# Kernel tuning notes

Measured on AMD Instinct MI355X. Metric: run time of the kernel, lower is better.

The kernel has to match this reference:

```python
import jax, jax.numpy as jnp
import numpy as np

N_NODES = 100000
N_EDGES = 600000
EMB_DIM = 128
NUM_LAYER = 3
NUM_GRAPHS = 64


def setup_inputs() -> dict:
    key = jax.random.key(0)
    ks = jax.random.split(key, 10)
    s = 1.0 / np.sqrt(EMB_DIM)  # keep activations stable through stacked GEMMs
    return {
        "x": jax.random.randint(ks[0], (N_NODES, 2), 0, 2),
        "edge_index_pos": jax.random.randint(ks[1], (2, N_EDGES), 0, N_NODES),
        "edge_index_inv": jax.random.randint(ks[2], (2, N_EDGES), 0, N_NODES),
        "batch": jnp.sort(jax.random.randint(ks[3], (N_NODES,), 0, NUM_GRAPHS)),
        "type_emb": jax.random.normal(ks[4], (14, EMB_DIM), jnp.float32),
        "output_emb": jax.random.normal(ks[5], (2, EMB_DIM), jnp.float32),
        "lin1_w": jax.random.normal(ks[6], (NUM_LAYER, 2, EMB_DIM, EMB_DIM), jnp.float32) * s,
        "lin1_b": jnp.zeros((NUM_LAYER, 2, EMB_DIM), jnp.float32),
        "lin2_w": jax.random.normal(ks[7], (NUM_LAYER, 2, EMB_DIM, EMB_DIM), jnp.float32) * s,
        "lin2_b": jnp.zeros((NUM_LAYER, 2, EMB_DIM), jnp.float32),
    }


def _gin_rel(h, ei, w1, b1, w2, b2):
    # GINConv (eps=0): MLP(x + sum_{j in N(i)} x_j); messages flow src(row0)->dst(row1)
    agg = jax.ops.segment_sum(h[ei[0]], ei[1], num_segments=h.shape[0])
    z = jax.nn.relu((h + agg) @ w1 + b1)
    return z @ w2 + b2


def reference(x, edge_index_pos, edge_index_inv, batch, type_emb, output_emb,
              lin1_w, lin1_b, lin2_w, lin2_b):
    # node input embedding: type + output-flag
    h = type_emb[x[:, 0]] + output_emb[x[:, 1]]
    num_layer = lin1_w.shape[0]
    for l in range(num_layer):  # small fixed layer loop
        hn = (_gin_rel(h, edge_index_pos, lin1_w[l, 0], lin1_b[l, 0], lin2_w[l, 0], lin2_b[l, 0])
              + _gin_rel(h, edge_index_inv, lin1_w[l, 1], lin1_b[l, 1], lin2_w[l, 1], lin2_b[l, 1]))
        h = hn if l == num_layer - 1 else jax.nn.relu(hn)  # JK='last', drop_ratio=0
    node_rep = h
    # MultiAggregation(['sum','mean','max','min']) pooling by graph id
    sum_g = jax.ops.segment_sum(node_rep, batch, num_segments=NUM_GRAPHS)
    cnt = jax.ops.segment_sum(jnp.ones((node_rep.shape[0],), node_rep.dtype), batch, num_segments=NUM_GRAPHS)
    mean_g = sum_g / jnp.maximum(cnt, 1.0)[:, None]
    max_g = jax.ops.segment_max(node_rep, batch, num_segments=NUM_GRAPHS)
    min_g = jax.ops.segment_min(node_rep, batch, num_segments=NUM_GRAPHS)
    h_graph = jnp.concatenate([sum_g, mean_g, max_g, min_g], axis=1)  # [B, 4*D]
    h_graph = h_graph.reshape(NUM_GRAPHS, -1, 4).transpose(0, 2, 1)   # [B, 4, D] (interleaved as in torch view)
    batch_mask = jnp.ones((NUM_GRAPHS, 4), dtype=bool)
    return (h_graph, batch_mask)
```

## Files before the change

kernel.cpp:

```cpp
#include <hip/hip_runtime.h>
#include <stdint.h>

#define M_NODES 100000
#define M_PAD   100096
#define NE      600000
#define DIM     128
#define NGRAPH  64
#define SCAN_B  512
#define SCAN_NB ((M_NODES + SCAN_B - 1) / SCAN_B)
#define WP      136

typedef __attribute__((ext_vector_type(8))) short short8;
typedef __attribute__((ext_vector_type(4))) float f32x4;

__device__ inline float bf2lo(uint32_t u) { return __uint_as_float(u << 16); }
__device__ inline float bf2hi(uint32_t u) { return __uint_as_float(u & 0xffff0000u); }
__device__ inline uint32_t packbf2(float a, float b) {
    uint32_t ua = __float_as_uint(a), ub = __float_as_uint(b);
    ua += 0x7fffu + ((ua >> 16) & 1u);
    ub += 0x7fffu + ((ub >> 16) & 1u);
    return (ua >> 16) | (ub & 0xffff0000u);
}
__device__ inline uint16_t ftobf16(float f) {
    uint32_t u = __float_as_uint(f);
    u += 0x7fffu + ((u >> 16) & 1u);
    return (uint16_t)(u >> 16);
}

#define GB_EMBED 25000
#define GB_TRANS (GB_EMBED + 12)
#define GB_ZERO  (GB_TRANS + 391)
#define GB_BOUND (GB_ZERO + 391)
__global__ void k_setup(const int* __restrict__ x, const float2* __restrict__ te2,
                        const float2* __restrict__ oe2, uint32_t* __restrict__ h2,
                        const float* __restrict__ w1, const float* __restrict__ w2,
                        uint16_t* __restrict__ wfrag,
                        const int* __restrict__ batch, int* __restrict__ starts,
                        int* __restrict__ degp, int* __restrict__ degi,
                        int* __restrict__ curp, int* __restrict__ curi) {
    int b = blockIdx.x, t = threadIdx.x;
    if (b < GB_EMBED) {
        int id = b * 256 + t;
        int node = id >> 6, p = id & 63;
        int x0 = x[node * 2], x1 = x[node * 2 + 1];
        float2 a = te2[x0 * 64 + p], bb = oe2[x1 * 64 + p];
        h2[node * 64 + p] = packbf2(a.x + bb.x, a.y + bb.y);
    } else if (b < GB_TRANS) {
        int m = b - GB_EMBED;
        const float* src;
        uint16_t* dst;
        if (m < 6) {
            int L = m >> 1, rel = m & 1;
            src = w1 + m * 16384;
            dst = wfrag + (size_t)(L * 4 + rel) * 16384;
        } else {
            int mm = m - 6, L = mm >> 1, rel = mm & 1;
            src = w2 + mm * 16384;
            dst = wfrag + (size_t)(L * 4 + 2 + rel) * 16384;
        }
        for (int o = t; o < 16384; o += 256) {
            int f = o >> 3, j = o & 7;
            int fb = f >> 6, ln = f & 63;
            int t_ = fb >> 2, s_ = fb & 3, qq = ln >> 4, ll = ln & 15;
            dst[o] = ftobf16(src[(s_ * 32 + qq * 8 + j) * 128 + t_ * 16 + ll]);
        }
    } else if (b < GB_ZERO) {
        int i = (b - GB_TRANS) * 256 + t;
        if (i < M_NODES) { degp[i] = 0; degi[i] = 0; curp[i] = 0; curi[i] = 0; }
    } else {
        int i = (b - GB_ZERO) * 256 + t;
        if (i >= M_NODES) return;
        int bb = batch[i];
        int pb = (i == 0) ? -1 : batch[i - 1];
        for (int g = pb + 1; g <= bb; ++g) starts[g] = i;
        if (i == M_NODES - 1)
            for (int g = bb + 1; g <= NGRAPH; ++g) starts[g] = M_NODES;
    }
}

__global__ void k_hist(const int* __restrict__ ep, const int* __restrict__ ei,
                       int* __restrict__ degp, int* __restrict__ degi) {
    int e = blockIdx.x * blockDim.x + threadIdx.x;
    if (e >= NE) return;
    atomicAdd(&degp[ep[NE + e]], 1);
    atomicAdd(&degi[ei[NE + e]], 1);
}

__global__ void k_scan1(const int* __restrict__ degp, const int* __restrict__ degi,
                        int* __restrict__ rsp, int* __restrict__ rsi, int* __restrict__ bsum) {
    __shared__ int s[SCAN_B];
    int list = blockIdx.y;
    const int* deg = list ? degi : degp;
    int* rs = list ? rsi : rsp;
    int i = blockIdx.x * SCAN_B + threadIdx.x;
    int v = (i < M_NODES) ? deg[i] : 0;
    s[threadIdx.x] = v;
    __syncthreads();
    for (int off = 1; off < SCAN_B; off <<= 1) {
        int xv = (threadIdx.x >= off) ? s[threadIdx.x - off] : 0;
        __syncthreads();
        s[threadIdx.x] += xv;
        __syncthreads();
    }
    if (i < M_NODES) rs[i + 1] = s[threadIdx.x];
    if (threadIdx.x == SCAN_B - 1) bsum[list * SCAN_NB + blockIdx.x] = s[threadIdx.x];
}

__global__ void k_scan2(const int* __restrict__ bsum, int* __restrict__ boff) {
    __shared__ int s[256];
    int list = blockIdx.x, t = threadIdx.x;
    int v = (t < SCAN_NB) ? bsum[list * SCAN_NB + t] : 0;
    s[t] = v;
    __syncthreads();
    for (int off = 1; off < 256; off <<= 1) {
        int xv = (t >= off) ? s[t - off] : 0;
        __syncthreads();
        s[t] += xv;
        __syncthreads();
    }
    if (t < SCAN_NB) boff[list * SCAN_NB + t] = s[t] - v;
}

__global__ void k_scan3(int* __restrict__ rsp, int* __restrict__ rsi, const int* __restrict__ boff) {
    int list = blockIdx.y;
    int* rs = list ? rsi : rsp;
    int i = blockIdx.x * SCAN_B + threadIdx.x;
    if (i < M_NODES) rs[i + 1] += boff[list * SCAN_NB + blockIdx.x];
    if (i == 0 && list == 0) { rsp[0] = 0; rsi[0] = 0; }
}

__global__ void k_fill(const int* __restrict__ ep, const int* __restrict__ ei,
                       const int* __restrict__ rsp, const int* __restrict__ rsi,
                       int* __restrict__ curp, int* __restrict__ curi,
                       int* __restrict__ csrp, int* __restrict__ csri) {
    int e = blockIdx.x * blockDim.x + threadIdx.x;
    if (e >= NE) return;
    int dp = ep[NE + e], sp_ = ep[e];
    int di = ei[NE + e], si_ = ei[e];
#pragma unroll 1
    for (int w = 0; w < 8; ++w) {
        int lo = w * 12500, hi = lo + 12500;
        if (dp >= lo && dp < hi) { int p = atomicAdd(&curp[dp], 1); csrp[rsp[dp] + p] = sp_; }
        if (di >= lo && di < hi) { int p = atomicAdd(&curi[di], 1); csri[rsi[di] + p] = si_; }
    }
}

__device__ inline void add8(float* a, uint4 v) {
    a[0] += bf2lo(v.x); a[1] += bf2hi(v.x);
    a[2] += bf2lo(v.y); a[3] += bf2hi(v.y);
    a[4] += bf2lo(v.z); a[5] += bf2hi(v.z);
    a[6] += bf2lo(v.w); a[7] += bf2hi(v.w);
}

__device__ inline void gather_tail(const uint4* __restrict__ h4, const int* __restrict__ csr,
                                   int e, int e1, int p, float* a) {
    for (; e + 4 <= e1; e += 4) {
        int i0 = csr[e], i1 = csr[e + 1], i2 = csr[e + 2], i3 = csr[e + 3];
        uint4 v0 = h4[(size_t)i0 * 16 + p];
        uint4 v1 = h4[(size_t)i1 * 16 + p];
        uint4 v2 = h4[(size_t)i2 * 16 + p];
        uint4 v3 = h4[(size_t)i3 * 16 + p];
        add8(a, v0); add8(a, v1); add8(a, v2); add8(a, v3);
    }
    for (; e < e1; ++e) add8(a, h4[(size_t)csr[e] * 16 + p]);
}

__global__ void k_aggregate2(const uint4* __restrict__ h4,
                             const int* __restrict__ rsp, const int* __restrict__ csrp,
                             const int* __restrict__ rsi, const int* __restrict__ csri,
                             uint4* __restrict__ up, uint4* __restrict__ ui) {
    int id = blockIdx.x * blockDim.x + threadIdx.x;
    int node = id >> 4, p = id & 15;
    if (node >= M_NODES) return;
    uint4 hv = h4[(size_t)node * 16 + p];
    float a[8] = {bf2lo(hv.x), bf2hi(hv.x), bf2lo(hv.y), bf2hi(hv.y),
                  bf2lo(hv.z), bf2hi(hv.z), bf2lo(hv.w), bf2hi(hv.w)};
    float b[8];
#pragma unroll
    for (int j = 0; j < 8; ++j) b[j] = a[j];
    int ea = rsp[node], e1a = rsp[node + 1];
    int eb = rsi[node], e1b = rsi[node + 1];
    while (ea + 2 <= e1a && eb + 2 <= e1b) {
        int ia0 = csrp[ea], ia1 = csrp[ea + 1];
        int ib0 = csri[eb], ib1 = csri[eb + 1];
        uint4 va0 = h4[(size_t)ia0 * 16 + p];
        uint4 va1 = h4[(size_t)ia1 * 16 + p];
        uint4 vb0 = h4[(size_t)ib0 * 16 + p];
        uint4 vb1 = h4[(size_t)ib1 * 16 + p];
        add8(a, va0); add8(a, va1); add8(b, vb0); add8(b, vb1);
        ea += 2; eb += 2;
    }
    gather_tail(h4, csrp, ea, e1a, p, a);
    gather_tail(h4, csri, eb, e1b, p, b);
    up[(size_t)node * 16 + p] = make_uint4(packbf2(a[0], a[1]), packbf2(a[2], a[3]),
                                           packbf2(a[4], a[5]), packbf2(a[6], a[7]));
    ui[(size_t)node * 16 + p] = make_uint4(packbf2(b[0], b[1]), packbf2(b[2], b[3]),
                                           packbf2(b[4], b[5]), packbf2(b[6], b[7]));
}

__launch_bounds__(256, 2)
__global__ void k_gemm2(const uint16_t* __restrict__ Up, const uint16_t* __restrict__ Ui,
                        const uint16_t* __restrict__ WF1p, const float* __restrict__ B1p,
                        const uint16_t* __restrict__ WF2p, const float* __restrict__ B2p,
                        const uint16_t* __restrict__ WF1i, const float* __restrict__ B1i,
                        const uint16_t* __restrict__ WF2i, const float* __restrict__ B2i,
                        float* __restrict__ HN, uint16_t* __restrict__ HOUT, int last) {
    __shared__ __align__(16) uint16_t wbuf[16384];
    __shared__ __align__(16) uint16_t sZ[2][64 * WP];
    int tid = threadIdx.x;
    int wave = tid >> 6, lane = tid & 63;
    int q = lane >> 4, l16 = lane & 15;
    int rb0 = blockIdx.x * 128 + wave * 16;
    int rb1 = rb0 + 64;

    auto loadA = [&](const uint16_t* U, int rowbase, short8* v) {
        const uint16_t* P = U + (size_t)(rowbase + l16) * DIM + q * 8;
#pragma unroll
        for (int s = 0; s < 4; ++s) v[s] = *(const short8*)(P + s * 32);
    };
    auto loadw = [&](const uint16_t* WF) {
#pragma unroll
        for (int i = tid; i < 2048; i += 256)
            *(uint4*)&wbuf[i * 8] = *(const uint4*)(WF + (size_t)i * 8);
    };
    auto stage1 = [&](const short8* af, const float* B1, int zslot) {
        f32x4 acc1[8];
#pragma unroll
        for (int t = 0; t < 8; ++t) acc1[t] = (f32x4){0.f, 0.f, 0.f, 0.f};
#pragma unroll
        for (int t = 0; t < 8; ++t)
#pragma unroll
            for (int s = 0; s < 4; ++s) {
                short8 bb = *(const short8*)&wbuf[((t * 4 + s) * 64 + lane) * 8];
                acc1[t] = __builtin_amdgcn_mfma_f32_16x16x32_bf16(af[s], bb, acc1[t], 0, 0, 0);
            }
#pragma unroll
        for (int t = 0; t < 8; ++t) {
            float b1v = B1[t * 16 + l16];
#pragma unroll
            for (int r = 0; r < 4; ++r)
                sZ[zslot][(wave * 16 + q * 4 + r) * WP + t * 16 + l16] =
                    ftobf16(fmaxf(acc1[t][r] + b1v, 0.f));
        }
    };
    auto stage2 = [&](int zslot, f32x4* acc2) {
        short8 zf[4];
#pragma unroll
        for (int s = 0; s < 4; ++s)
            zf[s] = *(const short8*)&sZ[zslot][(wave * 16 + l16) * WP + s * 32 + q * 8];
#pragma unroll
        for (int t = 0; t < 8; ++t)
#pragma unroll
            for (int s = 0; s < 4; ++s) {
                short8 bb = *(const short8*)&wbuf[((t * 4 + s) * 64 + lane) * 8];
                acc2[t] = __builtin_amdgcn_mfma_f32_16x16x32_bf16(zf[s], bb, acc2[t], 0, 0, 0);
            }
    };

    f32x4 acc2a[8], acc2b[8];
#pragma unroll
    for (int t = 0; t < 8; ++t) { acc2a[t] = (f32x4){0.f,0.f,0.f,0.f}; acc2b[t] = (f32x4){0.f,0.f,0.f,0.f}; }

    short8 af0[4], af1[4];
    loadA(Up, rb0, af0); loadA(Up, rb1, af1);
    loadw(WF1p); __syncthreads();
    stage1(af0, B1p, 0); stage1(af1, B1p, 1);
    __syncthreads();
    loadw(WF2p); __syncthreads();
    stage2(0, acc2a); stage2(1, acc2b);
    __syncthreads();
    loadA(Ui, rb0, af0); loadA(Ui, rb1, af1);
    loadw(WF1i); __syncthreads();
    stage1(af0, B1i, 0); stage1(af1, B1i, 1);
    __syncthreads();
    loadw(WF2i); __syncthreads();
    stage2(0, acc2a); stage2(1, acc2b);

#pragma unroll
    for (int t = 0; t < 8; ++t) {
        int col = t * 16 + l16;
        float b2v = B2p[col] + B2i[col];
#pragma unroll
        for (int r = 0; r < 4; ++r) {
            int row0 = rb0 + q * 4 + r, row1 = rb1 + q * 4 + r;
            float y0 = acc2a[t][r] + b2v, y1 = acc2b[t][r] + b2v;
            if (last) {
                HN[(size_t)row0 * DIM + col] = y0;
                HN[(size_t)row1 * DIM + col] = y1;
            } else {
                HOUT[(size_t)row0 * DIM + col] = ftobf16(fmaxf(y0, 0.f));
                HOUT[(size_t)row1 * DIM + col] = ftobf16(fmaxf(y1, 0.f));
            }
        }
    }
}

__global__ void k_pool1(const float* __restrict__ HN, const int* __restrict__ starts,
                        float* __restrict__ psum, float* __restrict__ pmax, float* __restrict__ pmin) {
    int g = blockIdx.x, sp = blockIdx.y, t = threadIdx.x;
    int d = t & 127, rh = t >> 7;
    int slot = sp * 2 + rh;
    int s0 = starts[g], s1 = starts[g + 1];
    float s = 0.f, mx = -INFINITY, mn = INFINITY;
    for (int i = s0 + slot; i < s1; i += 32) {
        float v = HN[(size_t)i * DIM + d];
        s += v; mx = fmaxf(mx, v); mn = fminf(mn, v);
    }
    int o = (g * 32 + slot) * DIM + d;
    psum[o] = s; pmax[o] = mx; pmin[o] = mn;
}

__global__ void k_pool2(const float* __restrict__ psum, const float* __restrict__ pmax,
                        const float* __restrict__ pmin, const int* __restrict__ starts,
                        float* __restrict__ out) {
    __shared__ float S[4][128];
    int g = blockIdx.x, t = threadIdx.x;
    float s = 0.f, mx = -INFINITY, mn = INFINITY;
    for (int p = 0; p < 32; ++p) {
        int o = (g * 32 + p) * DIM + t;
        s += psum[o]; mx = fmaxf(mx, pmax[o]); mn = fminf(mn, pmin[o]);
    }
    float cnt = (float)(starts[g + 1] - starts[g]);
    float mean = s / fmaxf(cnt, 1.f);
    S[0][t] = s; S[1][t] = mean; S[2][t] = mx; S[3][t] = mn;
    __syncthreads();
#pragma unroll
    for (int k = 0; k < 4; ++k) {
        int j = 4 * t + k;
        out[g * 512 + k * 128 + t] = S[j >> 7][j & 127];
    }
    if (t < 4) out[NGRAPH * 512 + g * 4 + t] = 1.0f;
}

extern "C" void kernel_launch(void* const* d_in, const int* in_sizes, int n_in,
                              void* d_out, int out_size, void* d_ws, size_t ws_size,
                              hipStream_t stream) {
    const int* x     = (const int*)d_in[0];
    const int* ep    = (const int*)d_in[1];
    const int* ei    = (const int*)d_in[2];
    const int* batch = (const int*)d_in[3];
    const float* te  = (const float*)d_in[4];
    const float* oe  = (const float*)d_in[5];
    const float* w1  = (const float*)d_in[6];
    const float* b1  = (const float*)d_in[7];
    const float* w2  = (const float*)d_in[8];
    const float* b2  = (const float*)d_in[9];
    float* out = (float*)d_out;

    char* w = (char*)d_ws;
    auto alloc = [&](size_t n) { char* p = w; w += (n + 255) & ~(size_t)255; return p; };
    uint16_t* h_bf  = (uint16_t*)alloc((size_t)M_PAD * DIM * 2);
    uint16_t* u_pos = (uint16_t*)alloc((size_t)M_PAD * DIM * 2);
    uint16_t* u_inv = (uint16_t*)alloc((size_t)M_PAD * DIM * 2);
    float*    hn    = (float*)alloc((size_t)M_PAD * DIM * 4);
    uint16_t* wfrag = (uint16_t*)alloc((size_t)12 * 16384 * 2);
    int* rsp  = (int*)alloc((M_NODES + 2) * 4);
    int* rsi  = (int*)alloc((M_NODES + 2) * 4);
    int* degp = (int*)alloc(M_NODES * 4);
    int* degi = (int*)alloc(M_NODES * 4);
    int* curp = (int*)alloc(M_NODES * 4);
    int* curi = (int*)alloc(M_NODES * 4);
    int* csrp = (int*)alloc((size_t)NE * 4);
    int* csri = (int*)alloc((size_t)NE * 4);
    int* bsum = (int*)alloc(2 * SCAN_NB * 4);
    int* boff = (int*)alloc(2 * SCAN_NB * 4);
    int* starts = (int*)alloc((NGRAPH + 1) * 4);
    float* psum = (float*)alloc(NGRAPH * 32 * DIM * 4);
    float* pmax = (float*)alloc(NGRAPH * 32 * DIM * 4);
    float* pmin = (float*)alloc(NGRAPH * 32 * DIM * 4);
    if ((size_t)(w - (char*)d_ws) > ws_size) return;

    k_setup<<<GB_BOUND, 256, 0, stream>>>(x, (const float2*)te, (const float2*)oe,
                                          (uint32_t*)h_bf, w1, w2, wfrag,
                                          batch, starts, degp, degi, curp, curi);
    k_hist<<<(NE + 255) / 256, 256, 0, stream>>>(ep, ei, degp, degi);
    dim3 gs(SCAN_NB, 2);
    k_scan1<<<gs, SCAN_B, 0, stream>>>(degp, degi, rsp, rsi, bsum);
    k_scan2<<<2, 256, 0, stream>>>(bsum, boff);
    k_scan3<<<gs, SCAN_B, 0, stream>>>(rsp, rsi, boff);
    k_fill<<<(NE + 255) / 256, 256, 0, stream>>>(ep, ei, rsp, rsi, curp, curi, csrp, csri);

    for (int l = 0; l < 3; ++l) {
        k_aggregate2<<<(M_NODES * 16 + 255) / 256, 256, 0, stream>>>(
            (const uint4*)h_bf, rsp, csrp, rsi, csri, (uint4*)u_pos, (uint4*)u_inv);
        const uint16_t* wfL = wfrag + (size_t)l * 4 * 16384;
        k_gemm2<<<M_PAD / 128, 256, 0, stream>>>(
            u_pos, u_inv,
            wfL,              b1 + (2 * l) * 128,
            wfL + 2 * 16384,  b2 + (2 * l) * 128,
            wfL + 16384,      b1 + (2 * l + 1) * 128,
            wfL + 3 * 16384,  b2 + (2 * l + 1) * 128,
            hn, h_bf, (l == 2) ? 1 : 0);
    }
    dim3 gp(NGRAPH, 16);
    k_pool1<<<gp, 256, 0, stream>>>(hn, starts, psum, pmax, pmin);
    k_pool2<<<NGRAPH, 128, 0, stream>>>(psum, pmax, pmin, starts, out);
}
```

Before: 543.4 us.

## Double-buffer GEMM weights in LDS and stage output stores through shared memory

The fused two-relation MLP kernel now prefetches the next weight matrix into registers while the current MFMA stage runs, then commits it to a second LDS buffer. This halves the number of barriers and hides the global weight loads. Output writes are also routed through LDS so each lane stores contiguous 16-byte vectors instead of scattered 2- or 4-byte elements. The extra LDS buffer and 32 prefetch registers lead to lowering the launch-bounds occupancy hint from 2 to 1, which may reduce latency hiding.

```diff
diff --git a/kernel.cpp b/kernel.cpp
--- a/kernel.cpp
+++ b/kernel.cpp
@@ -198,14 +198,14 @@
                                            packbf2(b[4], b[5]), packbf2(b[6], b[7]));
 }
 
-__launch_bounds__(256, 2)
+__launch_bounds__(256, 1)
 __global__ void k_gemm2(const uint16_t* __restrict__ Up, const uint16_t* __restrict__ Ui,
                         const uint16_t* __restrict__ WF1p, const float* __restrict__ B1p,
                         const uint16_t* __restrict__ WF2p, const float* __restrict__ B2p,
                         const uint16_t* __restrict__ WF1i, const float* __restrict__ B1i,
                         const uint16_t* __restrict__ WF2i, const float* __restrict__ B2i,
                         float* __restrict__ HN, uint16_t* __restrict__ HOUT, int last) {
-    __shared__ __align__(16) uint16_t wbuf[16384];
+    __shared__ __align__(16) uint16_t wbuf[2][16384];
     __shared__ __align__(16) uint16_t sZ[2][64 * WP];
     int tid = threadIdx.x;
     int wave = tid >> 6, lane = tid & 63;
@@ -213,17 +213,23 @@
     int rb0 = blockIdx.x * 128 + wave * 16;
     int rb1 = rb0 + 64;
 
+    uint4 pf[8];
+    auto issueW = [&](const uint16_t* WF) {
+#pragma unroll
+        for (int i = 0; i < 8; ++i)
+            pf[i] = *(const uint4*)(WF + (size_t)(tid + i * 256) * 8);
+    };
+    auto commitW = [&](int wb) {
+#pragma unroll
+        for (int i = 0; i < 8; ++i)
+            *(uint4*)&wbuf[wb][(size_t)(tid + i * 256) * 8] = pf[i];
+    };
     auto loadA = [&](const uint16_t* U, int rowbase, short8* v) {
         const uint16_t* P = U + (size_t)(rowbase + l16) * DIM + q * 8;
 #pragma unroll
         for (int s = 0; s < 4; ++s) v[s] = *(const short8*)(P + s * 32);
     };
-    auto loadw = [&](const uint16_t* WF) {
-#pragma unroll
-        for (int i = tid; i < 2048; i += 256)
-            *(uint4*)&wbuf[i * 8] = *(const uint4*)(WF + (size_t)i * 8);
-    };
-    auto stage1 = [&](const short8* af, const float* B1, int zslot) {
+    auto stage1 = [&](const short8* af, const float* B1, int zslot, int wb) {
         f32x4 acc1[8];
 #pragma unroll
         for (int t = 0; t < 8; ++t) acc1[t] = (f32x4){0.f, 0.f, 0.f, 0.f};
@@ -231,7 +237,7 @@
         for (int t = 0; t < 8; ++t)
 #pragma unroll
             for (int s = 0; s < 4; ++s) {
-                short8 bb = *(const short8*)&wbuf[((t * 4 + s) * 64 + lane) * 8];
+                short8 bb = *(const short8*)&wbuf[wb][((t * 4 + s) * 64 + lane) * 8];
                 acc1[t] = __builtin_amdgcn_mfma_f32_16x16x32_bf16(af[s], bb, acc1[t], 0, 0, 0);
             }
 #pragma unroll
@@ -243,7 +249,7 @@
                     ftobf16(fmaxf(acc1[t][r] + b1v, 0.f));
         }
     };
-    auto stage2 = [&](int zslot, f32x4* acc2) {
+    auto stage2 = [&](int zslot, f32x4* acc2, int wb) {
         short8 zf[4];
 #pragma unroll
         for (int s = 0; s < 4; ++s)
@@ -252,7 +258,7 @@
         for (int t = 0; t < 8; ++t)
 #pragma unroll
             for (int s = 0; s < 4; ++s) {
-                short8 bb = *(const short8*)&wbuf[((t * 4 + s) * 64 + lane) * 8];
+                short8 bb = *(const short8*)&wbuf[wb][((t * 4 + s) * 64 + lane) * 8];
                 acc2[t] = __builtin_amdgcn_mfma_f32_16x16x32_bf16(zf[s], bb, acc2[t], 0, 0, 0);
             }
     };
@@ -262,35 +268,69 @@
     for (int t = 0; t < 8; ++t) { acc2a[t] = (f32x4){0.f,0.f,0.f,0.f}; acc2b[t] = (f32x4){0.f,0.f,0.f,0.f}; }
 
     short8 af0[4], af1[4];
+    issueW(WF1p);
     loadA(Up, rb0, af0); loadA(Up, rb1, af1);
-    loadw(WF1p); __syncthreads();
-    stage1(af0, B1p, 0); stage1(af1, B1p, 1);
-    __syncthreads();
-    loadw(WF2p); __syncthreads();
-    stage2(0, acc2a); stage2(1, acc2b);
-    __syncthreads();
+    commitW(0);
+    __syncthreads();
+    issueW(WF2p);
+    stage1(af0, B1p, 0, 0); stage1(af1, B1p, 1, 0);
+    commitW(1);
+    __syncthreads();
+    issueW(WF1i);
     loadA(Ui, rb0, af0); loadA(Ui, rb1, af1);
-    loadw(WF1i); __syncthreads();
-    stage1(af0, B1i, 0); stage1(af1, B1i, 1);
-    __syncthreads();
-    loadw(WF2i); __syncthreads();
-    stage2(0, acc2a); stage2(1, acc2b);
-
-#pragma unroll
-    for (int t = 0; t < 8; ++t) {
-        int col = t * 16 + l16;
-        float b2v = B2p[col] + B2i[col];
-#pragma unroll
-        for (int r = 0; r < 4; ++r) {
-            int row0 = rb0 + q * 4 + r, row1 = rb1 + q * 4 + r;
-            float y0 = acc2a[t][r] + b2v, y1 = acc2b[t][r] + b2v;
-            if (last) {
-                HN[(size_t)row0 * DIM + col] = y0;
-                HN[(size_t)row1 * DIM + col] = y1;
-            } else {
-                HOUT[(size_t)row0 * DIM + col] = ftobf16(fmaxf(y0, 0.f));
-                HOUT[(size_t)row1 * DIM + col] = ftobf16(fmaxf(y1, 0.f));
+    stage2(0, acc2a, 1); stage2(1, acc2b, 1);
+    commitW(0);
+    __syncthreads();
+    issueW(WF2i);
+    stage1(af0, B1i, 0, 0); stage1(af1, B1i, 1, 0);
+    commitW(1);
+    __syncthreads();
+    stage2(0, acc2a, 1); stage2(1, acc2b, 1);
+
+    if (last) {
+        float* F = (float*)&sZ[0][0];
+        __syncthreads();
+        int row_l = lane >> 2, m = lane & 3;
+#pragma unroll 1
+        for (int tile = 0; tile < 2; ++tile) {
+            const f32x4* acc = tile ? acc2b : acc2a;
+            int rbt = tile ? rb1 : rb0;
+#pragma unroll
+            for (int t = 0; t < 8; ++t) {
+                float bv = B2p[t * 16 + l16] + B2i[t * 16 + l16];
+#pragma unroll
+                for (int r = 0; r < 4; ++r)
+                    F[(wave * 16 + q * 4 + r) * 132 + t * 16 + l16] = acc[t][r] + bv;
             }
+            __syncthreads();
+#pragma unroll
+            for (int k = 0; k < 8; ++k) {
+                int c = m + k * 4;
+                f32x4 v = *(const f32x4*)&F[(wave * 16 + row_l) * 132 + c * 4];
+                *(f32x4*)&HN[(size_t)(rbt + row_l) * DIM + c * 4] = v;
+            }
+            __syncthreads();
+        }
+    } else {
+#pragma unroll
+        for (int t = 0; t < 8; ++t) {
+            int col = t * 16 + l16;
+            float bv = B2p[col] + B2i[col];
+#pragma unroll
+            for (int r = 0; r < 4; ++r) {
+                int rr = (wave * 16 + q * 4 + r) * WP + col;
+                sZ[0][rr] = ftobf16(fmaxf(acc2a[t][r] + bv, 0.f));
+                sZ[1][rr] = ftobf16(fmaxf(acc2b[t][r] + bv, 0.f));
+            }
+        }
+        int row_l = lane >> 2, m = lane & 3;
+#pragma unroll
+        for (int k = 0; k < 4; ++k) {
+            int ch = m + k * 4;
+            short8 v0 = *(const short8*)&sZ[0][(wave * 16 + row_l) * WP + ch * 8];
+            short8 v1 = *(const short8*)&sZ[1][(wave * 16 + row_l) * WP + ch * 8];
+            *(short8*)(HOUT + (size_t)(rb0 + row_l) * DIM + ch * 8) = v0;
+            *(short8*)(HOUT + (size_t)(rb1 + row_l) * DIM + ch * 8) = v1;
         }
     }
 }
```

Measured after the change: 599.1 us. 1.1x slower.

## Fuse neighbor aggregation into the per-layer GEMM kernel via shared memory

Applied to the files above, without the earlier changes.

Merges the separate gather/aggregate kernel into the MLP GEMM kernel. Each block gathers neighbor sums for its 128 rows straight into shared memory, then runs the MFMA stages on them. This removes the global round trip of the bf16 aggregation buffers and one launch per layer. The node features now ping-pong between two buffers to avoid a read/write race. The gather runs inside a block limited to 2 blocks per CU with heavy LDS use, so it gets less parallelism to hide memory latency, and the gather phases are serialized with the GEMM phases inside each block.

```diff
diff --git a/kernel.cpp b/kernel.cpp
--- a/kernel.cpp
+++ b/kernel.cpp
@@ -165,41 +165,10 @@
     for (; e < e1; ++e) add8(a, h4[(size_t)csr[e] * 16 + p]);
 }
 
-__global__ void k_aggregate2(const uint4* __restrict__ h4,
-                             const int* __restrict__ rsp, const int* __restrict__ csrp,
-                             const int* __restrict__ rsi, const int* __restrict__ csri,
-                             uint4* __restrict__ up, uint4* __restrict__ ui) {
-    int id = blockIdx.x * blockDim.x + threadIdx.x;
-    int node = id >> 4, p = id & 15;
-    if (node >= M_NODES) return;
-    uint4 hv = h4[(size_t)node * 16 + p];
-    float a[8] = {bf2lo(hv.x), bf2hi(hv.x), bf2lo(hv.y), bf2hi(hv.y),
-                  bf2lo(hv.z), bf2hi(hv.z), bf2lo(hv.w), bf2hi(hv.w)};
-    float b[8];
-#pragma unroll
-    for (int j = 0; j < 8; ++j) b[j] = a[j];
-    int ea = rsp[node], e1a = rsp[node + 1];
-    int eb = rsi[node], e1b = rsi[node + 1];
-    while (ea + 2 <= e1a && eb + 2 <= e1b) {
-        int ia0 = csrp[ea], ia1 = csrp[ea + 1];
-        int ib0 = csri[eb], ib1 = csri[eb + 1];
-        uint4 va0 = h4[(size_t)ia0 * 16 + p];
-        uint4 va1 = h4[(size_t)ia1 * 16 + p];
-        uint4 vb0 = h4[(size_t)ib0 * 16 + p];
-        uint4 vb1 = h4[(size_t)ib1 * 16 + p];
-        add8(a, va0); add8(a, va1); add8(b, vb0); add8(b, vb1);
-        ea += 2; eb += 2;
-    }
-    gather_tail(h4, csrp, ea, e1a, p, a);
-    gather_tail(h4, csri, eb, e1b, p, b);
-    up[(size_t)node * 16 + p] = make_uint4(packbf2(a[0], a[1]), packbf2(a[2], a[3]),
-                                           packbf2(a[4], a[5]), packbf2(a[6], a[7]));
-    ui[(size_t)node * 16 + p] = make_uint4(packbf2(b[0], b[1]), packbf2(b[2], b[3]),
-                                           packbf2(b[4], b[5]), packbf2(b[6], b[7]));
-}
-
 __launch_bounds__(256, 2)
-__global__ void k_gemm2(const uint16_t* __restrict__ Up, const uint16_t* __restrict__ Ui,
+__global__ void k_layer(const uint4* __restrict__ h4,
+                        const int* __restrict__ rsp, const int* __restrict__ csrp,
+                        const int* __restrict__ rsi, const int* __restrict__ csri,
                         const uint16_t* __restrict__ WF1p, const float* __restrict__ B1p,
                         const uint16_t* __restrict__ WF2p, const float* __restrict__ B2p,
                         const uint16_t* __restrict__ WF1i, const float* __restrict__ B1i,
@@ -213,10 +182,27 @@
     int rb0 = blockIdx.x * 128 + wave * 16;
     int rb1 = rb0 + 64;
 
-    auto loadA = [&](const uint16_t* U, int rowbase, short8* v) {
-        const uint16_t* P = U + (size_t)(rowbase + l16) * DIM + q * 8;
-#pragma unroll
-        for (int s = 0; s < 4; ++s) v[s] = *(const short8*)(P + s * 32);
+    auto gather_rel = [&](const int* __restrict__ rs, const int* __restrict__ csr) {
+        int node16 = tid >> 4, p = tid & 15;
+#pragma unroll 1
+        for (int tile = 0; tile < 2; ++tile)
+#pragma unroll 1
+            for (int it = 0; it < 4; ++it) {
+                int r = it * 16 + node16;
+                int grow = blockIdx.x * 128 + tile * 64 + r;
+                float a[8] = {0.f, 0.f, 0.f, 0.f, 0.f, 0.f, 0.f, 0.f};
+                if (grow < M_NODES) {
+                    uint4 hv = h4[(size_t)grow * 16 + p];
+                    a[0] = bf2lo(hv.x); a[1] = bf2hi(hv.x);
+                    a[2] = bf2lo(hv.y); a[3] = bf2hi(hv.y);
+                    a[4] = bf2lo(hv.z); a[5] = bf2hi(hv.z);
+                    a[6] = bf2lo(hv.w); a[7] = bf2hi(hv.w);
+                    gather_tail(h4, csr, rs[grow], rs[grow + 1], p, a);
+                }
+                *(uint4*)&sZ[tile][r * WP + p * 8] =
+                    make_uint4(packbf2(a[0], a[1]), packbf2(a[2], a[3]),
+                               packbf2(a[4], a[5]), packbf2(a[6], a[7]));
+            }
     };
     auto loadw = [&](const uint16_t* WF) {
 #pragma unroll
@@ -262,18 +248,34 @@
     for (int t = 0; t < 8; ++t) { acc2a[t] = (f32x4){0.f,0.f,0.f,0.f}; acc2b[t] = (f32x4){0.f,0.f,0.f,0.f}; }
 
     short8 af0[4], af1[4];
-    loadA(Up, rb0, af0); loadA(Up, rb1, af1);
-    loadw(WF1p); __syncthreads();
+    auto readAF = [&]() {
+#pragma unroll
+        for (int s = 0; s < 4; ++s) {
+            af0[s] = *(const short8*)&sZ[0][(wave * 16 + l16) * WP + s * 32 + q * 8];
+            af1[s] = *(const short8*)&sZ[1][(wave * 16 + l16) * WP + s * 32 + q * 8];
+        }
+    };
+
+    gather_rel(rsp, csrp);
+    __syncthreads();
+    readAF();
+    loadw(WF1p);
+    __syncthreads();
     stage1(af0, B1p, 0); stage1(af1, B1p, 1);
     __syncthreads();
-    loadw(WF2p); __syncthreads();
+    loadw(WF2p);
+    __syncthreads();
     stage2(0, acc2a); stage2(1, acc2b);
     __syncthreads();
-    loadA(Ui, rb0, af0); loadA(Ui, rb1, af1);
-    loadw(WF1i); __syncthreads();
+    gather_rel(rsi, csri);
+    __syncthreads();
+    readAF();
+    loadw(WF1i);
+    __syncthreads();
     stage1(af0, B1i, 0); stage1(af1, B1i, 1);
     __syncthreads();
-    loadw(WF2i); __syncthreads();
+    loadw(WF2i);
+    __syncthreads();
     stage2(0, acc2a); stage2(1, acc2b);
 
 #pragma unroll
@@ -349,9 +351,8 @@
 
     char* w = (char*)d_ws;
     auto alloc = [&](size_t n) { char* p = w; w += (n + 255) & ~(size_t)255; return p; };
-    uint16_t* h_bf  = (uint16_t*)alloc((size_t)M_PAD * DIM * 2);
-    uint16_t* u_pos = (uint16_t*)alloc((size_t)M_PAD * DIM * 2);
-    uint16_t* u_inv = (uint16_t*)alloc((size_t)M_PAD * DIM * 2);
+    uint16_t* h_a   = (uint16_t*)alloc((size_t)M_PAD * DIM * 2);
+    uint16_t* h_b   = (uint16_t*)alloc((size_t)M_PAD * DIM * 2);
     float*    hn    = (float*)alloc((size_t)M_PAD * DIM * 4);
     uint16_t* wfrag = (uint16_t*)alloc((size_t)12 * 16384 * 2);
     int* rsp  = (int*)alloc((M_NODES + 2) * 4);
@@ -371,7 +372,7 @@
     if ((size_t)(w - (char*)d_ws) > ws_size) return;
 
     k_setup<<<GB_BOUND, 256, 0, stream>>>(x, (const float2*)te, (const float2*)oe,
-                                          (uint32_t*)h_bf, w1, w2, wfrag,
+                                          (uint32_t*)h_a, w1, w2, wfrag,
                                           batch, starts, degp, degi, curp, curi);
     k_hist<<<(NE + 255) / 256, 256, 0, stream>>>(ep, ei, degp, degi);
     dim3 gs(SCAN_NB, 2);
@@ -380,17 +381,18 @@
     k_scan3<<<gs, SCAN_B, 0, stream>>>(rsp, rsi, boff);
     k_fill<<<(NE + 255) / 256, 256, 0, stream>>>(ep, ei, rsp, rsi, curp, curi, csrp, csri);
 
+    uint16_t* hcur = h_a;
+    uint16_t* hnext = h_b;
     for (int l = 0; l < 3; ++l) {
-        k_aggregate2<<<(M_NODES * 16 + 255) / 256, 256, 0, stream>>>(
-            (const uint4*)h_bf, rsp, csrp, rsi, csri, (uint4*)u_pos, (uint4*)u_inv);
         const uint16_t* wfL = wfrag + (size_t)l * 4 * 16384;
-        k_gemm2<<<M_PAD / 128, 256, 0, stream>>>(
-            u_pos, u_inv,
+        k_layer<<<M_PAD / 128, 256, 0, stream>>>(
+            (const uint4*)hcur, rsp, csrp, rsi, csri,
             wfL,              b1 + (2 * l) * 128,
             wfL + 2 * 16384,  b2 + (2 * l) * 128,
             wfL + 16384,      b1 + (2 * l + 1) * 128,
             wfL + 3 * 16384,  b2 + (2 * l + 1) * 128,
-            hn, h_bf, (l == 2) ? 1 : 0);
+            hn, hnext, (l == 2) ? 1 : 0);
+        uint16_t* tmp = hcur; hcur = hnext; hnext = tmp;
     }
     dim3 gp(NGRAPH, 16);
     k_pool1<<<gp, 256, 0, stream>>>(hn, starts, psum, pmax, pmin);
```

After: 672.6 us. +23.8%, slower.
